# Performance work log

Measured on AMD Instinct MI355X. Metric: run time of the kernel, lower is better.

Reference implementation:

```python
import jax, jax.numpy as jnp
import numpy as np

B, C, H, W = 4, 256, 160, 160
N = 512
REID = 128
NUM_LAYERS = 2
BINS = 7          # adaptive_avg_pool2d target (7,7)
EPS_BN = 1e-5
EPS_NORM = 1e-12  # torch F.normalize eps


def setup_inputs() -> dict:
    key = jax.random.key(0)
    ks = jax.random.split(key, 8)
    x = jax.random.normal(ks[0], (B, C, H, W), jnp.float32)
    # valid normalized boxes: x1,y1 in [0,0.7], w,h in [0.1,0.3]
    xy1 = jax.random.uniform(ks[1], (B, N, 2), minval=0.0, maxval=0.7)
    wh = jax.random.uniform(ks[2], (B, N, 2), minval=0.1, maxval=0.3)
    bboxes = jnp.concatenate([xy1, jnp.minimum(xy1 + wh, 1.0)], axis=-1)
    # conv stack params (kaiming-ish init), BN in eval mode with running stats
    conv_w = jax.random.normal(ks[3], (NUM_LAYERS, C, C, 3, 3), jnp.float32) * np.sqrt(2.0 / (C * 9)).astype(np.float32)
    conv_b = jnp.zeros((NUM_LAYERS, C), jnp.float32)
    bn_gamma = jnp.ones((NUM_LAYERS, C), jnp.float32)
    bn_beta = jnp.zeros((NUM_LAYERS, C), jnp.float32)
    bn_mean = jnp.zeros((NUM_LAYERS, C), jnp.float32)
    bn_var = jnp.ones((NUM_LAYERS, C), jnp.float32)
    # reid_embedding MLP: Linear(C, C//2) -> ReLU -> Dropout(eval) -> Linear(C//2, REID)
    w1 = jax.random.normal(ks[4], (C // 2, C), jnp.float32) * 0.01
    b1 = jnp.zeros((C // 2,), jnp.float32)
    w2 = jax.random.normal(ks[5], (REID, C // 2), jnp.float32) * 0.01
    b2 = jnp.zeros((REID,), jnp.float32)
    return dict(x=x, bboxes=bboxes, conv_w=conv_w, conv_b=conv_b,
                bn_gamma=bn_gamma, bn_beta=bn_beta, bn_mean=bn_mean, bn_var=bn_var,
                w1=w1, b1=b1, w2=w2, b2=b2)


def _conv_bn_relu(x, w, b, gamma, beta, mean, var):
    y = jax.lax.conv_general_dilated(
        x, w, window_strides=(1, 1), padding=((1, 1), (1, 1)),
        dimension_numbers=('NCHW', 'OIHW', 'NCHW')) + b[None, :, None, None]
    scale = (gamma / jnp.sqrt(var + EPS_BN))[None, :, None, None]
    y = (y - mean[None, :, None, None]) * scale + beta[None, :, None, None]
    return jax.nn.relu(y)


def _roi_pool(S, box):
    # S: (C, H+1, W+1) integral image of the feature map; box: (4,) = x1,y1,x2,y2 in [0,1]
    x1 = jnp.clip(jnp.floor(box[0] * W).astype(jnp.int32), 0, W)
    y1 = jnp.clip(jnp.floor(box[1] * H).astype(jnp.int32), 0, H)
    x2 = jnp.clip(jnp.floor(box[2] * W).astype(jnp.int32), 0, W)
    y2 = jnp.clip(jnp.floor(box[3] * H).astype(jnp.int32), 0, H)
    valid = (x2 > x1) & (y2 > y1)
    hl = jnp.maximum(y2 - y1, 1)
    wl = jnp.maximum(x2 - x1, 1)
    i = jnp.arange(BINS)
    # PyTorch adaptive_avg_pool2d binning: [floor(i*L/B), ceil((i+1)*L/B))
    hs = y1 + (i * hl) // BINS
    he = y1 + ((i + 1) * hl + BINS - 1) // BINS
    ws = x1 + (i * wl) // BINS
    we = x1 + ((i + 1) * wl + BINS - 1) // BINS
    # bin sums via integral image -> (C, 7, 7)
    s = (S[:, he[:, None], we[None, :]] - S[:, hs[:, None], we[None, :]]
         - S[:, he[:, None], ws[None, :]] + S[:, hs[:, None], ws[None, :]])
    area = ((he - hs)[:, None] * (we - ws)[None, :]).astype(S.dtype)
    # adaptive 7x7 avg pool, then global avg pool over the 7x7 grid
    pooled = jnp.mean(s / area, axis=(1, 2))  # (C,)
    return pooled, valid


def reference(x, bboxes, conv_w, conv_b, bn_gamma, bn_beta, bn_mean, bn_var, w1, b1, w2, b2):
    f = x
    for l in range(NUM_LAYERS):
        f = _conv_bn_relu(f, conv_w[l], conv_b[l], bn_gamma[l], bn_beta[l], bn_mean[l], bn_var[l])
    # integral image, zero-padded: S[b,c,y,x] = sum of f[b,c,:y,:x] -> (B, C, H+1, W+1)
    S = jnp.pad(jnp.cumsum(jnp.cumsum(f, axis=2), axis=3), ((0, 0), (0, 0), (1, 0), (1, 0)))
    pooled, valid = jax.vmap(jax.vmap(_roi_pool, in_axes=(None, 0)), in_axes=(0, 0))(S, bboxes)
    # reid_embedding MLP (dropout is identity in eval)
    h = jax.nn.relu(jnp.einsum('bnc,hc->bnh', pooled, w1) + b1)
    feat = jnp.einsum('bnh,rh->bnr', h, w2) + b2
    feat = jnp.where(valid[..., None], feat, jnp.zeros((), feat.dtype))
    norm = jnp.maximum(jnp.linalg.norm(feat, axis=-1, keepdims=True), EPS_NORM)
    return feat / norm
```

## Files before the change

### kernel.cpp

```cpp
#include <hip/hip_runtime.h>
#include <hip/hip_bf16.h>

typedef __attribute__((ext_vector_type(8))) short s16x8;
typedef __attribute__((ext_vector_type(4))) float f32x4;


__device__ __forceinline__ void async_ld16(const void* g, void* l) {
  __builtin_amdgcn_global_load_lds(
      (const __attribute__((address_space(1))) void*)g,
      (__attribute__((address_space(3))) void*)l, 16, 0, 0);
}

__global__ __launch_bounds__(256) void zero_borders(__hip_bfloat16* __restrict__ xpad,
                                                    __hip_bfloat16* __restrict__ f1) {
  int bi = blockIdx.x;
  int buf = bi / 2576; int rem = bi - buf * 2576;
  int b = rem / 644;   int e = rem - b * 644;
  int y, x;
  if (e < 162)      { y = 0;           x = e; }
  else if (e < 324) { y = 161;         x = e - 162; }
  else if (e < 484) { y = e - 324 + 1; x = 0; }
  else              { y = e - 484 + 1; x = 161; }
  __hip_bfloat16* p = (buf ? f1 : xpad) + (((size_t)b * 162 + y) * 162 + x) * 256 + threadIdx.x;
  *p = __float2bfloat16(0.f);
}

__global__ __launch_bounds__(256) void nchw2nhwc(const float* __restrict__ x,
                                                 __hip_bfloat16* __restrict__ xpad) {
  __shared__ float tile[32][33];
  int blk = blockIdx.x;
  int xt = blk % 5;
  int ct = (blk / 5) & 7;
  int by = blk / 40;
  int b = by / 160, y = by - (by / 160) * 160;
  int tx = threadIdx.x, ty = threadIdx.y;
  const float* src = x + (((size_t)(b * 256 + ct * 32)) * 160 + y) * 160 + xt * 32 + tx;
#pragma unroll
  for (int k = 0; k < 4; k++) tile[ty * 4 + k][tx] = src[(size_t)(ty * 4 + k) * 25600];
  __syncthreads();
  __hip_bfloat16* dst = xpad + (((size_t)(b * 162 + y + 1)) * 162 + (xt * 32 + 1)) * 256 + ct * 32 + tx;
#pragma unroll
  for (int k = 0; k < 4; k++) {
    int xx = ty * 4 + k;
    dst[(size_t)xx * 256] = __float2bfloat16(tile[tx][xx]);
  }
}

__global__ __launch_bounds__(256) void pack_w(const float* __restrict__ cw,
                                              __hip_bfloat16* __restrict__ wpk) {
  int t = blockIdx.x * 256 + threadIdx.x;
  int ci = t & 255, co = (t >> 8) & 255, rest = t >> 16;
  int tap = rest % 9, l = rest / 9;
  int dy = tap / 3, dx = tap - dy * 3;
  float v = cw[((((size_t)l * 256 + co) * 256 + ci) * 3 + dy) * 3 + dx];
  wpk[(((size_t)l * 9 + tap) * 256 + co) * 256 + ci] = __float2bfloat16(v);
}

__global__ void prep_bn(const float* __restrict__ cb, const float* __restrict__ g,
                        const float* __restrict__ bt, const float* __restrict__ mn,
                        const float* __restrict__ vr, float* __restrict__ ab) {
  int t = blockIdx.x * 256 + threadIdx.x;
  float a = g[t] / sqrtf(vr[t] + 1e-5f);
  ab[t] = a;
  ab[512 + t] = (cb[t] - mn[t]) * a + bt[t];
}

__global__ __launch_bounds__(256) void pack_mlp(const float* __restrict__ w1,
                                                const float* __restrict__ w2,
                                                float* __restrict__ w1t,
                                                float* __restrict__ w2t) {
  int t = blockIdx.x * 256 + threadIdx.x;
  if (t < 32768) {
    int h = t >> 8, k = t & 255;
    w1t[k * 128 + h] = w1[h * 256 + k];
  } else {
    int u = t - 32768;
    int r = u >> 7, k = u & 127;
    w2t[k * 128 + r] = w2[r * 128 + k];
  }
}

__global__ __launch_bounds__(512, 2) void conv_bn_relu(
    const __hip_bfloat16* __restrict__ inp, __hip_bfloat16* __restrict__ outp,
    const __hip_bfloat16* __restrict__ wpk,
    const float* __restrict__ alpha, const float* __restrict__ beff) {
  __shared__ __align__(16) short As[2 * 256 * 64];
  __shared__ __align__(16) short Bs[2 * 256 * 64];
  const int t = threadIdx.x;
  const int mtile = ((blockIdx.x & 7) * 50) + (blockIdx.x >> 3);
  const int l = t & 63;
  const int wv = t >> 6;
  const int lr = l & 15, lq = l >> 4;
  const int wm = wv >> 2, wn = wv & 3;

  const int srow = t >> 3;
  const int koff = (((t & 7) ^ (srow & 7)) << 3);
  const short* inS = (const short*)inp;
  const short* wS = (const short*)wpk;
  long abase[4];
#pragma unroll
  for (int i = 0; i < 4; i++) {
    int p = mtile * 256 + i * 64 + srow;
    int b = p / 25600; int r = p - b * 25600; int y = r / 160; int x = r - y * 160;
    abase[i] = (((long)b * 162 + y) * 162 + x) * 256 + koff;
  }
  const long bbase = ((long)srow) * 256 + koff;

  auto stage = [&](int v) {
    const int tap = v >> 2, kc = v & 3;
    const int dy = tap / 3, dx = tap - dy * 3;
    const long aoff = ((long)(dy * 162 + dx)) * 256 + kc * 64;
    const long boff = (long)tap * 65536 + kc * 64;
    short* ad = As + (v & 1) * 16384 + t * 8;
    short* bd = Bs + (v & 1) * 16384 + t * 8;
#pragma unroll
    for (int i = 0; i < 4; i++)
      async_ld16(inS + abase[i] + aoff, ad + i * 4096);
#pragma unroll
    for (int i = 0; i < 4; i++)
      async_ld16(wS + bbase + boff + (long)i * 16384, bd + i * 4096);
  };

  f32x4 acc[8][4];
#pragma unroll
  for (int i = 0; i < 8; i++)
#pragma unroll
    for (int j = 0; j < 4; j++) acc[i][j] = (f32x4){0.f, 0.f, 0.f, 0.f};

  stage(0);
  __syncthreads();

#pragma unroll 2
  for (int u = 0; u < 36; ++u) {
    if (u < 35) stage(u + 1);
    const short* Ab = As + (u & 1) * 16384;
    const short* Bb = Bs + (u & 1) * 16384;
#pragma unroll
    for (int kk = 0; kk < 2; ++kk) {
      const int ps = (((kk << 2) | lq) ^ (lr & 7)) << 3;
      s16x8 av[8], bv[4];
#pragma unroll
      for (int mi = 0; mi < 8; ++mi)
        av[mi] = *(const s16x8*)&Ab[(wm * 128 + mi * 16 + lr) * 64 + ps];
#pragma unroll
      for (int ni = 0; ni < 4; ++ni)
        bv[ni] = *(const s16x8*)&Bb[(wn * 64 + ni * 16 + lr) * 64 + ps];
      __builtin_amdgcn_s_setprio(1);
#pragma unroll
      for (int mi = 0; mi < 8; ++mi)
#pragma unroll
        for (int ni = 0; ni < 4; ++ni)
          acc[mi][ni] = __builtin_amdgcn_mfma_f32_16x16x32_bf16(av[mi], bv[ni], acc[mi][ni], 0, 0, 0);
      __builtin_amdgcn_s_setprio(0);
    }
    __syncthreads();
  }

  float al[4], be_[4];
#pragma unroll
  for (int ni = 0; ni < 4; ++ni) {
    int co = wn * 64 + ni * 16 + lr;
    al[ni] = alpha[co];
    be_[ni] = beff[co];
  }
#pragma unroll
  for (int mi = 0; mi < 8; ++mi) {
    int prow = mtile * 256 + wm * 128 + mi * 16 + lq * 4;
#pragma unroll
    for (int j = 0; j < 4; ++j) {
      int p = prow + j;
      int b = p / 25600; int r = p - b * 25600; int y = r / 160; int x = r - y * 160;
      long ob = (((long)b * 162 + (y + 1)) * 162 + (x + 1)) * 256 + wn * 64;
#pragma unroll
      for (int ni = 0; ni < 4; ++ni) {
        float v = acc[mi][ni][j] * al[ni] + be_[ni];
        outp[ob + ni * 16 + lr] = __float2bfloat16(fmaxf(v, 0.f));
      }
    }
  }
}

__global__ __launch_bounds__(256) void cumsum_w(const __hip_bfloat16* __restrict__ f2,
                                                float* __restrict__ S) {
  int row = blockIdx.x * 2 + (threadIdx.x >> 7);
  int b = row / 160, y = row - (row / 160) * 160;
  int cp = threadIdx.x & 127;
  const unsigned* src =
      (const unsigned*)((const short*)f2 + (((size_t)b * 162 + y + 1) * 162 + 1) * 256) + cp;
  float2* dst = (float2*)(S + (((size_t)b * 161 + y + 1) * 161) * 256) + cp;
  dst[0] = float2{0.f, 0.f};
  float r0 = 0.f, r1 = 0.f;
  for (int x4 = 0; x4 < 160; x4 += 4) {
    unsigned v[4];
#pragma unroll
    for (int k = 0; k < 4; k++) v[k] = src[(size_t)(x4 + k) * 128];
#pragma unroll
    for (int k = 0; k < 4; k++) {
      r0 += __uint_as_float((v[k] & 0xffffu) << 16);
      r1 += __uint_as_float(v[k] & 0xffff0000u);
      dst[(size_t)(x4 + k + 1) * 128] = float2{r0, r1};
    }
  }
}

__global__ __launch_bounds__(256) void cumsum_h(float* __restrict__ S) {
  int bi = blockIdx.x;
  int b = bi / 161, q = bi - (bi / 161) * 161;
  int c = threadIdx.x;
  float* col = S + (((size_t)b * 161) * 161 + q) * 256 + c;
  const size_t ys = (size_t)161 * 256;
  col[0] = 0.f;
  float run = 0.f;
  for (int y0 = 1; y0 <= 160; y0 += 8) {
    float v[8];
#pragma unroll
    for (int k = 0; k < 8; k++) v[k] = col[(size_t)(y0 + k) * ys];
#pragma unroll
    for (int k = 0; k < 8; k++) { run += v[k]; col[(size_t)(y0 + k) * ys] = run; }
  }
}

__global__ __launch_bounds__(256) void roi_pool(const float* __restrict__ S,
                                                const float* __restrict__ bbox,
                                                float* __restrict__ pooled,
                                                int* __restrict__ valid) {
  int bn = blockIdx.x;
  int b = bn >> 9;
  int c = threadIdx.x;
  float bx1 = bbox[bn * 4 + 0], by1 = bbox[bn * 4 + 1];
  float bx2 = bbox[bn * 4 + 2], by2 = bbox[bn * 4 + 3];
  int x1 = min(max((int)floorf(bx1 * 160.f), 0), 160);
  int y1 = min(max((int)floorf(by1 * 160.f), 0), 160);
  int x2 = min(max((int)floorf(bx2 * 160.f), 0), 160);
  int y2 = min(max((int)floorf(by2 * 160.f), 0), 160);
  int vld = (x2 > x1 && y2 > y1) ? 1 : 0;
  int hl = max(y2 - y1, 1), wl = max(x2 - x1, 1);
  int hs[7], he[7], ws_[7], we_[7];
  float rh[7], rw[7];
#pragma unroll
  for (int i = 0; i < 7; i++) {
    hs[i] = y1 + (i * hl) / 7;
    he[i] = y1 + ((i + 1) * hl + 6) / 7;
    rh[i] = 1.f / (float)(he[i] - hs[i]);
    ws_[i] = x1 + (i * wl) / 7;
    we_[i] = x1 + ((i + 1) * wl + 6) / 7;
    rw[i] = 1.f / (float)(we_[i] - ws_[i]);
  }
  const float* Sb = S + (size_t)b * 161 * 161 * 256 + c;
  float acc = 0.f;
#pragma unroll
  for (int i = 0; i < 7; i++) {
    const float* rE = Sb + (size_t)he[i] * (161 * 256);
    const float* rS = Sb + (size_t)hs[i] * (161 * 256);
#pragma unroll
    for (int j = 0; j < 7; j++) {
      size_t qe = (size_t)we_[j] * 256, qs = (size_t)ws_[j] * 256;
      float s = rE[qe] - rS[qe] - rE[qs] + rS[qs];
      acc += s * (rh[i] * rw[j]);
    }
  }
  pooled[(size_t)bn * 256 + c] = acc * (1.f / 49.f);
  if (c == 0) valid[bn] = vld;
}

__global__ __launch_bounds__(128) void mlp_norm(const float* __restrict__ pooled,
                                                const int* __restrict__ valid,
                                                const float* __restrict__ w1t,
                                                const float* __restrict__ b1,
                                                const float* __restrict__ w2t,
                                                const float* __restrict__ b2,
                                                float* __restrict__ out) {
  int bn = blockIdx.x;
  int t = threadIdx.x;
  __shared__ float pl[256];
  __shared__ float hh[128];
  __shared__ float red[2];
  pl[t] = pooled[(size_t)bn * 256 + t];
  pl[t + 128] = pooled[(size_t)bn * 256 + 128 + t];
  __syncthreads();
  float a = b1[t];
#pragma unroll 8
  for (int k = 0; k < 256; k++) a += w1t[k * 128 + t] * pl[k];
  hh[t] = fmaxf(a, 0.f);
  __syncthreads();
  float f = b2[t];
#pragma unroll 8
  for (int k = 0; k < 128; k++) f += w2t[k * 128 + t] * hh[k];
  if (!valid[bn]) f = 0.f;
  float ss = f * f;
#pragma unroll
  for (int off = 32; off > 0; off >>= 1) ss += __shfl_xor(ss, off);
  if ((t & 63) == 0) red[t >> 6] = ss;
  __syncthreads();
  float nrm = fmaxf(sqrtf(red[0] + red[1]), 1e-12f);
  out[(size_t)bn * 128 + t] = f / nrm;
}

extern "C" void kernel_launch(void* const* d_in, const int* in_sizes, int n_in,
                              void* d_out, int out_size, void* d_ws, size_t ws_size,
                              hipStream_t stream) {
  const float* x = (const float*)d_in[0];
  const float* bboxes = (const float*)d_in[1];
  const float* conv_w = (const float*)d_in[2];
  const float* conv_b = (const float*)d_in[3];
  const float* bn_g = (const float*)d_in[4];
  const float* bn_b = (const float*)d_in[5];
  const float* bn_m = (const float*)d_in[6];
  const float* bn_v = (const float*)d_in[7];
  const float* w1 = (const float*)d_in[8];
  const float* b1 = (const float*)d_in[9];
  const float* w2 = (const float*)d_in[10];
  const float* b2 = (const float*)d_in[11];

  char* ws = (char*)d_ws;
  const size_t PADB = (size_t)4 * 162 * 162 * 256 * 2;
  const size_t WPKB = (size_t)2 * 9 * 256 * 256 * 2;
  const size_t SB = (size_t)4 * 161 * 161 * 256 * 4;
  const size_t PLB = (size_t)4 * 512 * 256 * 4;

  __hip_bfloat16* xpad = (__hip_bfloat16*)(ws);
  __hip_bfloat16* f1 = (__hip_bfloat16*)(ws + PADB);
  __hip_bfloat16* wpk = (__hip_bfloat16*)(ws + 2 * PADB);
  float* abuf = (float*)(ws + 2 * PADB + WPKB);
  float* S = (float*)(ws + 2 * PADB + WPKB + 4096);
  float* pooled = (float*)(ws + 2 * PADB + WPKB + 4096 + SB);
  int* valid = (int*)(ws + 2 * PADB + WPKB + 4096 + SB + PLB);
  float* w1t = (float*)(ws + 2 * PADB + WPKB + 4096 + SB + PLB + 8192);
  float* w2t = w1t + 32768;

  zero_borders<<<5152, 256, 0, stream>>>(xpad, f1);
  nchw2nhwc<<<25600, dim3(32, 8), 0, stream>>>(x, xpad);
  pack_w<<<4608, 256, 0, stream>>>(conv_w, wpk);
  prep_bn<<<2, 256, 0, stream>>>(conv_b, bn_g, bn_b, bn_m, bn_v, abuf);
  pack_mlp<<<192, 256, 0, stream>>>(w1, w2, w1t, w2t);

  conv_bn_relu<<<400, 512, 0, stream>>>(xpad, f1, wpk, abuf, abuf + 512);
  conv_bn_relu<<<400, 512, 0, stream>>>(f1, xpad, wpk + (size_t)9 * 256 * 256, abuf + 256, abuf + 768);

  cumsum_w<<<320, 256, 0, stream>>>(xpad, S);
  cumsum_h<<<644, 256, 0, stream>>>(S);
  roi_pool<<<2048, 256, 0, stream>>>(S, bboxes, pooled, valid);
  mlp_norm<<<2048, 128, 0, stream>>>(pooled, valid, w1t, b1, w2t, b2, (float*)d_out);
}
```

Before: 445.1 us.

## Interleave async loads with MFMA phases in conv GEMM main loop

Splits each K-step of the conv implicit GEMM into four phases of LDS reads plus MFMA blocks. Each phase issues a quarter of the next stage's global-to-LDS async loads, so memory traffic is spread across the compute rather than issued all at once. The B half of the stage after next is prefetched early, and explicit vmcnt waits and raw s_barrier replace __syncthreads. The cost is many more barriers per iteration and tricky correctness around the partial waits and buffer reuse.

```diff
diff --git a/kernel.cpp b/kernel.cpp
--- a/kernel.cpp
+++ b/kernel.cpp
@@ -10,6 +10,9 @@
       (const __attribute__((address_space(1))) void*)g,
       (__attribute__((address_space(3))) void*)l, 16, 0, 0);
 }
+
+#define CFENCE asm volatile("" ::: "memory")
+#define BARRIER do { CFENCE; __builtin_amdgcn_s_barrier(); CFENCE; } while (0)
 
 __global__ __launch_bounds__(256) void zero_borders(__hip_bfloat16* __restrict__ xpad,
                                                     __hip_bfloat16* __restrict__ f1) {
@@ -106,19 +109,20 @@
   }
   const long bbase = ((long)srow) * 256 + koff;
 
-  auto stage = [&](int v) {
+  auto stageA = [&](int v, int h) {
     const int tap = v >> 2, kc = v & 3;
     const int dy = tap / 3, dx = tap - dy * 3;
     const long aoff = ((long)(dy * 162 + dx)) * 256 + kc * 64;
+    short* d = As + (v & 1) * 16384 + h * 8192 + t * 8;
+    async_ld16(inS + abase[h * 2 + 0] + aoff, d);
+    async_ld16(inS + abase[h * 2 + 1] + aoff, d + 4096);
+  };
+  auto stageB = [&](int v, int h) {
+    const int tap = v >> 2, kc = v & 3;
     const long boff = (long)tap * 65536 + kc * 64;
-    short* ad = As + (v & 1) * 16384 + t * 8;
-    short* bd = Bs + (v & 1) * 16384 + t * 8;
-#pragma unroll
-    for (int i = 0; i < 4; i++)
-      async_ld16(inS + abase[i] + aoff, ad + i * 4096);
-#pragma unroll
-    for (int i = 0; i < 4; i++)
-      async_ld16(wS + bbase + boff + (long)i * 16384, bd + i * 4096);
+    short* d = Bs + (v & 1) * 16384 + h * 8192 + t * 8;
+    async_ld16(wS + bbase + (long)(h * 2 + 0) * 16384 + boff, d);
+    async_ld16(wS + bbase + (long)(h * 2 + 1) * 16384 + boff, d + 4096);
   };
 
   f32x4 acc[8][4];
@@ -127,33 +131,81 @@
 #pragma unroll
     for (int j = 0; j < 4; j++) acc[i][j] = (f32x4){0.f, 0.f, 0.f, 0.f};
 
-  stage(0);
-  __syncthreads();
-
-#pragma unroll 2
+  auto rdA = [&](const short* Ab, int mi, int kk) {
+    return *(const s16x8*)&Ab[(wm * 128 + mi * 16 + lr) * 64 +
+                              ((((kk << 2) | lq) ^ (lr & 7)) << 3)];
+  };
+  auto rdB = [&](const short* Bb, int ni, int kk) {
+    return *(const s16x8*)&Bb[(wn * 64 + ni * 16 + lr) * 64 +
+                              ((((kk << 2) | lq) ^ (lr & 7)) << 3)];
+  };
+
+  stageB(0, 0); stageB(0, 1); stageA(0, 0); stageA(0, 1); stageB(1, 0);
+  asm volatile("s_waitcnt vmcnt(2)" ::: "memory");
+  BARRIER;
+
+  s16x8 avlo[4], avhi[4], bv[4];
+#pragma unroll 1
   for (int u = 0; u < 36; ++u) {
-    if (u < 35) stage(u + 1);
     const short* Ab = As + (u & 1) * 16384;
     const short* Bb = Bs + (u & 1) * 16384;
 #pragma unroll
-    for (int kk = 0; kk < 2; ++kk) {
-      const int ps = (((kk << 2) | lq) ^ (lr & 7)) << 3;
-      s16x8 av[8], bv[4];
-#pragma unroll
-      for (int mi = 0; mi < 8; ++mi)
-        av[mi] = *(const s16x8*)&Ab[(wm * 128 + mi * 16 + lr) * 64 + ps];
+    for (int mi = 0; mi < 4; ++mi) avlo[mi] = rdA(Ab, mi, 0);
+#pragma unroll
+    for (int ni = 0; ni < 4; ++ni) bv[ni] = rdB(Bb, ni, 0);
+    if (u + 1 < 36) stageB(u + 1, 1);
+    BARRIER;
+    __builtin_amdgcn_s_setprio(1);
+#pragma unroll
+    for (int mi = 0; mi < 4; ++mi)
 #pragma unroll
       for (int ni = 0; ni < 4; ++ni)
-        bv[ni] = *(const s16x8*)&Bb[(wn * 64 + ni * 16 + lr) * 64 + ps];
-      __builtin_amdgcn_s_setprio(1);
-#pragma unroll
-      for (int mi = 0; mi < 8; ++mi)
-#pragma unroll
-        for (int ni = 0; ni < 4; ++ni)
-          acc[mi][ni] = __builtin_amdgcn_mfma_f32_16x16x32_bf16(av[mi], bv[ni], acc[mi][ni], 0, 0, 0);
-      __builtin_amdgcn_s_setprio(0);
+        acc[mi][ni] = __builtin_amdgcn_mfma_f32_16x16x32_bf16(avlo[mi], bv[ni], acc[mi][ni], 0, 0, 0);
+    __builtin_amdgcn_s_setprio(0);
+    BARRIER;
+#pragma unroll
+    for (int mi = 0; mi < 4; ++mi) avhi[mi] = rdA(Ab, mi + 4, 0);
+    if (u + 1 < 36) stageA(u + 1, 0);
+    BARRIER;
+    __builtin_amdgcn_s_setprio(1);
+#pragma unroll
+    for (int mi = 0; mi < 4; ++mi)
+#pragma unroll
+      for (int ni = 0; ni < 4; ++ni)
+        acc[mi + 4][ni] = __builtin_amdgcn_mfma_f32_16x16x32_bf16(avhi[mi], bv[ni], acc[mi + 4][ni], 0, 0, 0);
+    __builtin_amdgcn_s_setprio(0);
+    BARRIER;
+#pragma unroll
+    for (int mi = 0; mi < 4; ++mi) avlo[mi] = rdA(Ab, mi, 1);
+#pragma unroll
+    for (int ni = 0; ni < 4; ++ni) bv[ni] = rdB(Bb, ni, 1);
+    if (u + 1 < 36) stageA(u + 1, 1);
+    BARRIER;
+    __builtin_amdgcn_s_setprio(1);
+#pragma unroll
+    for (int mi = 0; mi < 4; ++mi)
+#pragma unroll
+      for (int ni = 0; ni < 4; ++ni)
+        acc[mi][ni] = __builtin_amdgcn_mfma_f32_16x16x32_bf16(avlo[mi], bv[ni], acc[mi][ni], 0, 0, 0);
+    __builtin_amdgcn_s_setprio(0);
+    BARRIER;
+#pragma unroll
+    for (int mi = 0; mi < 4; ++mi) avhi[mi] = rdA(Ab, mi + 4, 1);
+    if (u + 2 < 36) {
+      stageB(u + 2, 0);
+      asm volatile("s_waitcnt vmcnt(2)" ::: "memory");
+    } else if (u + 1 < 36) {
+      asm volatile("s_waitcnt vmcnt(0)" ::: "memory");
     }
-    __syncthreads();
+    BARRIER;
+    __builtin_amdgcn_s_setprio(1);
+#pragma unroll
+    for (int mi = 0; mi < 4; ++mi)
+#pragma unroll
+      for (int ni = 0; ni < 4; ++ni)
+        acc[mi + 4][ni] = __builtin_amdgcn_mfma_f32_16x16x32_bf16(avhi[mi], bv[ni], acc[mi + 4][ni], 0, 0, 0);
+    __builtin_amdgcn_s_setprio(0);
+    BARRIER;
   }
 
   float al[4], be_[4];
```

Result: faster. 429.3 us (-3.5%).
